# Optimization experiments

Hardware: AMD Instinct MI355X
Metric: run time of the kernel (lower is better)

## Reference

```python
import jax, jax.numpy as jnp
import numpy as np

B, S, HID, NH, HD = 2, 2048, 2048, 16, 128  # batch, seq, hidden, heads, head_dim
ROPE_BASE = 10000.0


def _rope_tables():
    inv_freq = 1.0 / (ROPE_BASE ** (np.arange(0, HD, 2, dtype=np.float64) / HD))
    freqs = np.outer(np.arange(S, dtype=np.float64), inv_freq)  # [S, HD/2]
    emb = np.concatenate([freqs, freqs], axis=-1)  # [S, HD]
    return (jnp.asarray(np.cos(emb), dtype=jnp.float32),
            jnp.asarray(np.sin(emb), dtype=jnp.float32))


def setup_inputs() -> dict:
    key = jax.random.key(0)
    k1, k2, k3 = jax.random.split(key, 3)
    x = jax.random.normal(k1, (B, S, HID), dtype=jnp.float32)
    # CastedLinear init std = 1/sqrt(in_features); plain normal is fine for a numeric reference
    w_qkv = jax.random.normal(k2, (3 * HID, HID), dtype=jnp.float32) * (1.0 / np.sqrt(HID))
    w_o = jax.random.normal(k3, (HID, HID), dtype=jnp.float32) * (1.0 / np.sqrt(HID))
    cos, sin = _rope_tables()
    return {"x": x, "w_qkv": w_qkv, "w_o": w_o, "cos": cos, "sin": sin}


def rotate_half(t):
    t1, t2 = jnp.split(t, 2, axis=-1)
    return jnp.concatenate([-t2, t1], axis=-1)


def reference(x, w_qkv, w_o, cos, sin):
    b, s, _ = x.shape
    # qkv_proj: F.linear -> x @ w_qkv.T
    qkv = jnp.einsum('bsi,oi->bso', x, w_qkv).reshape(b, s, 3, NH, HD)
    q, k, v = qkv[:, :, 0], qkv[:, :, 1], qkv[:, :, 2]  # [b, s, NH, HD]
    # RoPE: cos/sin [s, HD] broadcast over batch and heads
    c = cos[:, None, :]
    sn = sin[:, None, :]
    q = q * c + rotate_half(q) * sn
    k = k * c + rotate_half(k) * sn
    # [b, NH, s, HD]
    q = q.transpose(0, 2, 1, 3)
    k = k.transpose(0, 2, 1, 3)
    v = v.transpose(0, 2, 1, 3)
    scale = 1.0 / jnp.sqrt(jnp.asarray(HD, dtype=x.dtype))
    scores = jnp.einsum('bhqd,bhkd->bhqk', q, k) * scale
    causal_mask = jnp.triu(jnp.ones((s, s), dtype=bool), k=1)
    scores = jnp.where(causal_mask, jnp.asarray(-1e9, dtype=scores.dtype), scores)
    attn = jax.nn.softmax(scores, axis=-1)
    ctx = jnp.einsum('bhqk,bhkd->bhqd', attn, v)
    ctx = ctx.transpose(0, 2, 1, 3).reshape(b, s, HID)
    # o_proj: ctx @ w_o.T
    return jnp.einsum('bsi,oi->bso', ctx, w_o)
```

## Files before the change

### kernel.cpp

```cpp
#include <hip/hip_runtime.h>
#include <hip/hip_bf16.h>

typedef __bf16 bf16;
typedef __bf16 bf16x4 __attribute__((ext_vector_type(4)));
typedef __bf16 bf16x8 __attribute__((ext_vector_type(8)));
typedef float floatx4 __attribute__((ext_vector_type(4)));

#define Bb   2
#define Ss   2048
#define HID  2048
#define NH   16
#define HD   128
#define HG   8

typedef __attribute__((address_space(3))) unsigned int lds_u32;
typedef const __attribute__((address_space(1))) unsigned int gbl_u32;

__device__ __forceinline__ float b2f(bf16 h) {
    unsigned short u = __builtin_bit_cast(unsigned short, h);
    unsigned int x = ((unsigned int)u) << 16;
    return __builtin_bit_cast(float, x);
}
__device__ __forceinline__ bf16 f2b(float f) {
    __hip_bfloat16 t = __float2bfloat16(f);
    return __builtin_bit_cast(bf16, t);
}
__device__ __forceinline__ bf16x8 load8_f32(const float* p) {
    float4 u = *(const float4*)p;
    float4 v = *(const float4*)(p + 4);
    bf16x8 r;
    r[0] = f2b(u.x); r[1] = f2b(u.y); r[2] = f2b(u.z); r[3] = f2b(u.w);
    r[4] = f2b(v.x); r[5] = f2b(v.y); r[6] = f2b(v.z); r[7] = f2b(v.w);
    return r;
}
__device__ __forceinline__ void stage16(const bf16* g, bf16* l) {
    __builtin_amdgcn_global_load_lds((gbl_u32*)g, (lds_u32*)l, 16, 0, 0);
}


__global__ __launch_bounds__(256) void cvt_all(
    const float* __restrict__ x, const float* __restrict__ wq,
    const float* __restrict__ wo,
    bf16* __restrict__ xb, bf16* __restrict__ wqb, bf16* __restrict__ wob)
{
    int idx = blockIdx.x * 256 + threadIdx.x;
    int stride = gridDim.x * 256;
    for (int i = idx; i < 6291456; i += stride) {
        const float* in; bf16* out; int k;
        if (i < 2097152)      { in = x;  out = xb;  k = i; }
        else if (i < 5242880) { in = wq; out = wqb; k = i - 2097152; }
        else                  { in = wo; out = wob; k = i - 5242880; }
        float4 v = ((const float4*)in)[k];
        bf16x4 o; o[0] = f2b(v.x); o[1] = f2b(v.y); o[2] = f2b(v.z); o[3] = f2b(v.w);
        ((bf16x4*)out)[k] = o;
    }
}

__global__ __launch_bounds__(256) void qkv_gemm_rope(
    const bf16* __restrict__ xb, const bf16* __restrict__ wqb,
    const float* __restrict__ c0, const float* __restrict__ c1,
    bf16* __restrict__ q, bf16* __restrict__ k, bf16* __restrict__ vT)
{
    __shared__ __attribute__((aligned(16))) char smem[128 * 132 * 2];
    bf16* As = (bf16*)smem;
    bf16* Bs = (bf16*)(smem + 8192);
    typedef bf16 (*tile_t)[132];
    tile_t tile = (tile_t)smem;

    bool c0cos = (c0[0] > 0.5f);
    const float* cosT = c0cos ? c0 : c1;
    const float* sinT = c0cos ? c1 : c0;

    int tid = threadIdx.x, lane = tid & 63, w = tid >> 6;
    int l15 = lane & 15, quad = lane >> 4;
    int m0 = blockIdx.x * 128, n0 = blockIdx.y * 128;
    int mw = (w >> 1) * 64, nw = (w & 1) * 64;

    int srow = w * 32 + (lane >> 2);
    int scol = (lane & 3) * 8;
    const bf16* ga = xb  + (size_t)(m0 + srow) * HID + scol;
    const bf16* gb = wqb + (size_t)(n0 + srow) * HID + scol;
    bf16* la = As + w * 1024;
    bf16* lb = Bs + w * 1024;

    floatx4 acc[4][4] = {};
    for (int k0 = 0; k0 < HID; k0 += 32) {
        stage16(ga + k0,                    la);
        stage16(ga + (size_t)16 * HID + k0, la + 512);
        stage16(gb + k0,                    lb);
        stage16(gb + (size_t)16 * HID + k0, lb + 512);
        __syncthreads();
        bf16x8 a[4], b[4];
#pragma unroll
        for (int i = 0; i < 4; i++) {
            a[i] = *(const bf16x8*)&As[(mw + i * 16 + l15) * 32 + quad * 8];
            b[i] = *(const bf16x8*)&Bs[(nw + i * 16 + l15) * 32 + quad * 8];
        }
#pragma unroll
        for (int i = 0; i < 4; i++)
#pragma unroll
            for (int j = 0; j < 4; j++)
                acc[i][j] = __builtin_amdgcn_mfma_f32_16x16x32_bf16(a[i], b[j], acc[i][j], 0, 0, 0);
        __syncthreads();
    }

#pragma unroll
    for (int i = 0; i < 4; i++)
#pragma unroll
        for (int j = 0; j < 4; j++) {
            int row_l = mw + i * 16 + quad * 4;
            int col_l = nw + j * 16 + l15;
#pragma unroll
            for (int r = 0; r < 4; r++)
                tile[row_l + r][col_l] = f2b(acc[i][j][r]);
        }
    __syncthreads();

    int sec = blockIdx.y >> 4;
    int h   = blockIdx.y & 15;
    int bi  = m0 >> 11;
    int bh  = bi * NH + h;
    int sbase = m0 & (Ss - 1);

    if (sec == 2) {
        int d  = tid >> 1;
        int sh = (tid & 1) * 64;
        bf16* vrow = vT + ((size_t)bh * HD + d) * Ss + sbase + sh;
#pragma unroll 4
        for (int i = 0; i < 64; i += 4) {
            bf16x4 pk;
#pragma unroll
            for (int r = 0; r < 4; r++) pk[r] = tile[sh + i + r][d];
            *(bf16x4*)(vrow + i) = pk;
        }
    } else {
        bf16* dst = (sec == 0) ? q : k;
        int d  = tid & 63;
        int r0 = tid >> 6;
#pragma unroll 4
        for (int it = 0; it < 32; it++) {
            int row_l = it * 4 + r0;
            int s = sbase + row_l;
            float x1 = b2f(tile[row_l][d]);
            float x2 = b2f(tile[row_l][d + 64]);
            float cc1 = cosT[s * HD + d];
            float ss1 = sinT[s * HD + d];
            float cc2 = cosT[s * HD + d + 64];
            float ss2 = sinT[s * HD + d + 64];
            size_t o = ((size_t)bh * Ss + s) * HD + d;
            dst[o]      = f2b(x1 * cc1 - x2 * ss1);
            dst[o + 64] = f2b(x2 * cc2 + x1 * ss2);
        }
    }
}

#define ATTN_C1 (0.08838834764831845f * 1.44269504f)

#define STAGE_KV(BUF, KB)                                                        \
{                                                                                \
    const char* kg = kgbase + (size_t)(KB) * 256;                                \
    const char* vg = vgbase + (size_t)(KB) * 2;                                  \
    _Pragma("unroll")                                                            \
    for (int i = 0; i < 2; i++) {                                                \
        int P  = P0 + i * 1024;                                                  \
        int r  = P >> 8;                                                         \
        int cK = (P & 255) ^ ((r & 7) << 4);                                     \
        stage16((const bf16*)(kg + r * 256 + cK),                                \
                (bf16*)((char*)Kls[BUF] + wave * 2048 + i * 1024));              \
        int d  = P >> 6;                                                         \
        int cV = (P & 63) ^ (((d >> 1) & 3) << 4);                               \
        stage16((const bf16*)(vg + (size_t)d * 4096 + cV),                       \
                (bf16*)((char*)Vls[BUF] + wave * 2048 + i * 1024));              \
    }                                                                            \
}

__global__ __launch_bounds__(256, 4) void attn_full(
    const bf16* __restrict__ Q, const bf16* __restrict__ Kb, const bf16* __restrict__ VT,
    bf16* __restrict__ O)
{
    __shared__ __attribute__((aligned(16))) bf16 Kls[2][32 * 128];
    __shared__ __attribute__((aligned(16))) bf16 Vls[2][128 * 32];
    __shared__ bf16 pls[4][16][40];

    int id   = blockIdx.x;
    int xcd  = id & 7;
    int j    = id >> 3;
    int bh   = (xcd << 2) | (j & 3);
    int qt   = 31 - (j >> 2);

    int tid  = threadIdx.x;
    int wave = tid >> 6;
    int lane = tid & 63;
    int l15  = lane & 15;
    int quad = lane >> 4;

    int q0 = qt * 64 + wave * 16;
    int qg = q0 + l15;

    const char* kgbase = (const char*)(Kb + (size_t)bh * Ss * HD);
    const char* vgbase = (const char*)(VT + (size_t)bh * HD * Ss);
    int P0 = wave * 2048 + lane * 16;

    STAGE_KV(0, 0);

    const bf16* qptr = Q + ((size_t)bh * Ss + qg) * HD + quad * 8;
    bf16x8 qf[4];
#pragma unroll
    for (int s = 0; s < 4; s++) qf[s] = *(const bf16x8*)(qptr + s * 32);

    float m    = -1e30f;
    float bm   = 1.44269504e30f;
    float lsum = 0.0f;
    floatx4 ctx[8] = {};

    int nsteps = 2 * qt + 2;
    int buf = 0;
    __syncthreads();

    for (int st = 0; st < nsteps; st++) {
        int kb = st * 32;
        if (st + 1 < nsteps) {
            int bufn = buf ^ 1;
            STAGE_KV(bufn, kb + 32);
        }
        if (kb <= q0 + 15) {
            bool masked = (kb + 31 > q0);
            const char* kls = (const char*)Kls[buf];
            const char* vls = (const char*)Vls[buf];

            floatx4 s0 = {0.f,0.f,0.f,0.f}, s1 = {0.f,0.f,0.f,0.f};
            __builtin_amdgcn_s_setprio(1);
#pragma unroll
            for (int s = 0; s < 4; s++) {
                int c = (quad * 16 + s * 64) ^ ((l15 & 7) << 4);
                bf16x8 k0 = *(const bf16x8*)(kls + l15 * 256 + c);
                bf16x8 k1 = *(const bf16x8*)(kls + (l15 + 16) * 256 + c);
                s0 = __builtin_amdgcn_mfma_f32_16x16x32_bf16(k0, qf[s], s0, 0, 0, 0);
                s1 = __builtin_amdgcn_mfma_f32_16x16x32_bf16(k1, qf[s], s1, 0, 0, 0);
            }
            __builtin_amdgcn_s_setprio(0);

            float v0[4], v1[4];
#pragma unroll
            for (int r = 0; r < 4; r++) {
                int key0 = kb + quad * 4 + r;
                v0[r] = (masked && key0 > qg)      ? -1e9f : s0[r];
                v1[r] = (masked && key0 + 16 > qg) ? -1e9f : s1[r];
            }
            float lmax = fmaxf(fmaxf(fmaxf(v0[0], v0[1]), fmaxf(v0[2], v0[3])),
                               fmaxf(fmaxf(v1[0], v1[1]), fmaxf(v1[2], v1[3])));
            if (!__all(lmax * 0.08838834764831845f <= m + 8.0f)) {
                float tm = lmax;
                tm = fmaxf(tm, __shfl_xor(tm, 16));
                tm = fmaxf(tm, __shfl_xor(tm, 32));
                float tms  = tm * 0.08838834764831845f;
                float mnew = fmaxf(m, tms);
                float bmn  = -mnew * 1.44269504f;
                float alpha = __builtin_exp2f(bmn - bm);
                m = mnew; bm = bmn;
                lsum *= alpha;
#pragma unroll
                for (int t = 0; t < 8; t++) {
                    ctx[t][0] *= alpha; ctx[t][1] *= alpha;
                    ctx[t][2] *= alpha; ctx[t][3] *= alpha;
                }
            }
            bf16x4 pk0, pk1; float ts = 0.f;
#pragma unroll
            for (int r = 0; r < 4; r++) {
                float pe0 = __builtin_exp2f(__builtin_fmaf(v0[r], ATTN_C1, bm));
                float pe1 = __builtin_exp2f(__builtin_fmaf(v1[r], ATTN_C1, bm));
                ts += pe0 + pe1;
                pk0[r] = f2b(pe0); pk1[r] = f2b(pe1);
            }
            lsum += ts;
            *(bf16x4*)&pls[wave][l15][quad * 4]      = pk0;
            *(bf16x4*)&pls[wave][l15][16 + quad * 4] = pk1;
            bf16x8 pf = *(const bf16x8*)&pls[wave][l15][quad * 8];

            __builtin_amdgcn_s_setprio(1);
#pragma unroll
            for (int t = 0; t < 8; t++) {
                int row = t * 16 + l15;
                bf16x8 vf = *(const bf16x8*)(vls + row * 64 +
                                             ((quad * 16) ^ (((row >> 1) & 3) << 4)));
                ctx[t] = __builtin_amdgcn_mfma_f32_16x16x32_bf16(vf, pf, ctx[t], 0, 0, 0);
            }
            __builtin_amdgcn_s_setprio(0);
        }
        __syncthreads();
        buf ^= 1;
    }

    lsum += __shfl_xor(lsum, 16);
    lsum += __shfl_xor(lsum, 32);
    float inv = 1.0f / lsum;

    int bi = bh >> 4, h = bh & (NH - 1);
    bf16* op = O + ((size_t)(bi * Ss + qg)) * HID + h * HD;
#pragma unroll
    for (int t = 0; t < 8; t++) {
        bf16x4 ov;
#pragma unroll
        for (int r = 0; r < 4; r++) ov[r] = f2b(ctx[t][r] * inv);
        *(bf16x4*)(op + t * 16 + quad * 4) = ov;
    }
}

__global__ __launch_bounds__(256) void out_gemm(
    const bf16* __restrict__ A, const bf16* __restrict__ B, float* __restrict__ C)
{
    __shared__ bf16 As[128 * 32];
    __shared__ bf16 Bs[128 * 32];

    int tid = threadIdx.x, lane = tid & 63, w = tid >> 6;
    int l15 = lane & 15, quad = lane >> 4;
    int m0 = blockIdx.x * 128, n0 = blockIdx.y * 128;
    int mw = (w >> 1) * 64, nw = (w & 1) * 64;

    int srow = w * 32 + (lane >> 2);
    int scol = (lane & 3) * 8;
    const bf16* ga = A + (size_t)(m0 + srow) * HID + scol;
    const bf16* gb = B + (size_t)(n0 + srow) * HID + scol;
    bf16* la = As + w * 1024;
    bf16* lb = Bs + w * 1024;

    floatx4 acc[4][4] = {};
    for (int k0 = 0; k0 < HID; k0 += 32) {
        stage16(ga + k0,                    la);
        stage16(ga + (size_t)16 * HID + k0, la + 512);
        stage16(gb + k0,                    lb);
        stage16(gb + (size_t)16 * HID + k0, lb + 512);
        __syncthreads();
        bf16x8 a[4], b[4];
#pragma unroll
        for (int i = 0; i < 4; i++) {
            a[i] = *(const bf16x8*)&As[(mw + i * 16 + l15) * 32 + quad * 8];
            b[i] = *(const bf16x8*)&Bs[(nw + i * 16 + l15) * 32 + quad * 8];
        }
#pragma unroll
        for (int i = 0; i < 4; i++)
#pragma unroll
            for (int j = 0; j < 4; j++)
                acc[i][j] = __builtin_amdgcn_mfma_f32_16x16x32_bf16(a[i], b[j], acc[i][j], 0, 0, 0);
        __syncthreads();
    }

#pragma unroll
    for (int i = 0; i < 4; i++)
#pragma unroll
        for (int j = 0; j < 4; j++) {
            int row = m0 + mw + i * 16 + quad * 4;
            int col = n0 + nw + j * 16 + l15;
#pragma unroll
            for (int r = 0; r < 4; r++)
                C[(size_t)(row + r) * HID + col] = acc[i][j][r];
        }
}


__global__ __launch_bounds__(256) void qkv_rope_pass(
    const float* __restrict__ xb, const float* __restrict__ W,
    const float* __restrict__ c0, const float* __restrict__ c1,
    bf16* __restrict__ qc, bf16* __restrict__ kc, bf16* __restrict__ vc, int hg)
{
    __shared__ bf16 tile[128][132];
    bool c0cos = (c0[0] > 0.5f);
    const float* cosT = c0cos ? c0 : c1;
    const float* sinT = c0cos ? c1 : c0;

    int tid = threadIdx.x, lane = tid & 63, wave = tid >> 6;
    int l15 = lane & 15, quad = lane >> 4;
    int sec = blockIdx.y >> 3, hl = blockIdx.y & 7;
    int nbase = sec * (NH * HD) + (hg * HG + hl) * HD;
    int m0 = blockIdx.x * 128 + (wave >> 1) * 64;
    int n0l = (wave & 1) * 64;

    floatx4 acc[4][4] = {};
    const float* ap = xb + (size_t)(m0 + l15) * HID + quad * 8;
    const float* bp = W  + (size_t)(nbase + n0l + l15) * HID + quad * 8;
    for (int k0 = 0; k0 < HID; k0 += 32) {
        bf16x8 a[4], b[4];
#pragma unroll
        for (int i = 0; i < 4; i++) {
            a[i] = load8_f32(ap + (size_t)i * 16 * HID + k0);
            b[i] = load8_f32(bp + (size_t)i * 16 * HID + k0);
        }
#pragma unroll
        for (int i = 0; i < 4; i++)
#pragma unroll
            for (int j = 0; j < 4; j++)
                acc[i][j] = __builtin_amdgcn_mfma_f32_16x16x32_bf16(a[i], b[j], acc[i][j], 0, 0, 0);
    }
    int lr = (wave >> 1) * 64;
#pragma unroll
    for (int i = 0; i < 4; i++)
#pragma unroll
        for (int j = 0; j < 4; j++) {
            int row_l = lr + i * 16 + quad * 4;
            int col_l = n0l + j * 16 + l15;
#pragma unroll
            for (int r = 0; r < 4; r++)
                tile[row_l + r][col_l] = f2b(acc[i][j][r]);
        }
    __syncthreads();

    bf16* dst = (sec == 0) ? qc : (sec == 1) ? kc : vc;
    int d = tid & 63, r0 = tid >> 6;
#pragma unroll 4
    for (int it = 0; it < 32; it++) {
        int row_l = it * 4 + r0;
        int s = blockIdx.x * 128 + row_l;
        float x1 = b2f(tile[row_l][d]);
        float x2 = b2f(tile[row_l][d + 64]);
        size_t o = ((size_t)hl * Ss + s) * HD + d;
        if (sec == 2) { dst[o] = f2b(x1); dst[o + 64] = f2b(x2); }
        else {
            float cc1 = cosT[s * HD + d], ss1 = sinT[s * HD + d];
            float cc2 = cosT[s * HD + d + 64], ss2 = sinT[s * HD + d + 64];
            dst[o]      = f2b(x1 * cc1 - x2 * ss1);
            dst[o + 64] = f2b(x2 * cc2 + x1 * ss2);
        }
    }
}

__global__ __launch_bounds__(256) void attn_pass(
    const bf16* __restrict__ Q, const bf16* __restrict__ Kb, const bf16* __restrict__ Vb,
    bf16* __restrict__ Obase)
{
    __shared__ bf16 pls[4][16][40];
    int hl = blockIdx.x;
    int qt = (gridDim.y - 1) - blockIdx.y;
    int tid = threadIdx.x, wave = tid >> 6, lane = tid & 63;
    int l15 = lane & 15, quad = lane >> 4;
    int q0 = qt * 64 + wave * 16;
    int qg = q0 + l15;

    const bf16* qptr = Q + ((size_t)hl * Ss + qg) * HD + quad * 8;
    bf16x8 qf[4];
#pragma unroll
    for (int s = 0; s < 4; s++) qf[s] = *(const bf16x8*)(qptr + s * 32);

    float m = -1e30f, l = 0.0f;
    floatx4 ctx[8] = {};
    const float scale = 0.08838834764831845f;

    for (int kb = 0; kb <= q0 + 15; kb += 32) {
        floatx4 s0 = {0.f,0.f,0.f,0.f}, s1 = {0.f,0.f,0.f,0.f};
        const bf16* kp0 = Kb + ((size_t)hl * Ss + kb + l15) * HD + quad * 8;
        const bf16* kp1 = kp0 + (size_t)16 * HD;
#pragma unroll
        for (int s = 0; s < 4; s++) {
            bf16x8 k0 = *(const bf16x8*)(kp0 + s * 32);
            bf16x8 k1 = *(const bf16x8*)(kp1 + s * 32);
            s0 = __builtin_amdgcn_mfma_f32_16x16x32_bf16(k0, qf[s], s0, 0, 0, 0);
            s1 = __builtin_amdgcn_mfma_f32_16x16x32_bf16(k1, qf[s], s1, 0, 0, 0);
        }
        float v0[4], v1[4];
#pragma unroll
        for (int r = 0; r < 4; r++) {
            int key0 = kb + quad * 4 + r;
            v0[r] = (key0 > qg)      ? -1e9f : s0[r] * scale;
            v1[r] = (key0 + 16 > qg) ? -1e9f : s1[r] * scale;
        }
        float tmax = fmaxf(fmaxf(fmaxf(v0[0], v0[1]), fmaxf(v0[2], v0[3])),
                           fmaxf(fmaxf(v1[0], v1[1]), fmaxf(v1[2], v1[3])));
        tmax = fmaxf(tmax, __shfl_xor(tmax, 16));
        tmax = fmaxf(tmax, __shfl_xor(tmax, 32));
        float mnew = fmaxf(m, tmax);
        float alpha = __expf(m - mnew);
        float p0[4], p1[4], tsum = 0.0f;
#pragma unroll
        for (int r = 0; r < 4; r++) {
            p0[r] = __expf(v0[r] - mnew);
            p1[r] = __expf(v1[r] - mnew);
            tsum += p0[r] + p1[r];
        }
        tsum += __shfl_xor(tsum, 16);
        tsum += __shfl_xor(tsum, 32);
        l = l * alpha + tsum;
        m = mnew;
#pragma unroll
        for (int t = 0; t < 8; t++) {
            ctx[t][0] *= alpha; ctx[t][1] *= alpha;
            ctx[t][2] *= alpha; ctx[t][3] *= alpha;
        }
#pragma unroll
        for (int r = 0; r < 4; r++) {
            pls[wave][l15][quad * 4 + r]      = f2b(p0[r]);
            pls[wave][l15][16 + quad * 4 + r] = f2b(p1[r]);
        }
        bf16x8 pf = *(const bf16x8*)&pls[wave][l15][quad * 8];
        const short* vp = (const short*)(Vb + ((size_t)hl * Ss + kb) * HD);
#pragma unroll
        for (int t = 0; t < 8; t++) {
            bf16x8 vf;
#pragma unroll
            for (int j = 0; j < 8; j++) {
                short sv = vp[(size_t)(quad * 8 + j) * HD + t * 16 + l15];
                vf[j] = __builtin_bit_cast(bf16, sv);
            }
            ctx[t] = __builtin_amdgcn_mfma_f32_16x16x32_bf16(vf, pf, ctx[t], 0, 0, 0);
        }
    }
    float inv = 1.0f / l;
    bf16* op = Obase + (size_t)qg * HID + hl * HD;
#pragma unroll
    for (int t = 0; t < 8; t++) {
        bf16x4 ov;
#pragma unroll
        for (int r = 0; r < 4; r++) ov[r] = f2b(ctx[t][r] * inv);
        *(bf16x4*)(op + t * 16 + quad * 4) = ov;
    }
}

__global__ __launch_bounds__(256) void gemm_out_f32(
    const bf16* __restrict__ A, const float* __restrict__ B,
    float* __restrict__ C, int N, int K)
{
    int tid = threadIdx.x, lane = tid & 63, wave = tid >> 6;
    int l15 = lane & 15, quad = lane >> 4;
    int m0 = blockIdx.x * 128 + (wave >> 1) * 64;
    int n0 = blockIdx.y * 128 + (wave & 1) * 64;

    floatx4 acc[4][4] = {};
    const bf16*  ap = A + (size_t)(m0 + l15) * K + quad * 8;
    const float* bp = B + (size_t)(n0 + l15) * K + quad * 8;
    for (int k0 = 0; k0 < K; k0 += 32) {
        bf16x8 a[4], b[4];
#pragma unroll
        for (int i = 0; i < 4; i++) {
            a[i] = *(const bf16x8*)(ap + (size_t)i * 16 * K + k0);
            b[i] = load8_f32(bp + (size_t)i * 16 * K + k0);
        }
#pragma unroll
        for (int i = 0; i < 4; i++)
#pragma unroll
            for (int j = 0; j < 4; j++)
                acc[i][j] = __builtin_amdgcn_mfma_f32_16x16x32_bf16(a[i], b[j], acc[i][j], 0, 0, 0);
    }
#pragma unroll
    for (int i = 0; i < 4; i++)
#pragma unroll
        for (int j = 0; j < 4; j++) {
            int row = m0 + i * 16 + quad * 4;
            int col = n0 + j * 16 + l15;
#pragma unroll
            for (int r = 0; r < 4; r++)
                C[(size_t)(row + r) * N + col] = acc[i][j][r];
        }
}

extern "C" void kernel_launch(void* const* d_in, const int* in_sizes, int n_in,
                              void* d_out, int out_size, void* d_ws, size_t ws_size,
                              hipStream_t stream)
{
    const float *x = nullptr, *w_qkv = nullptr, *w_o = nullptr;
    const float *t0 = nullptr, *t1 = nullptr;
    for (int i = 0; i < n_in; i++) {
        const float* p = (const float*)d_in[i];
        if      (in_sizes[i] == 12582912) w_qkv = p;
        else if (in_sizes[i] ==  8388608) x     = p;
        else if (in_sizes[i] ==  4194304) w_o   = p;
        else if (in_sizes[i] ==   262144) { if (t0) t1 = p; else t0 = p; }
    }
    float* out = (float*)d_out;
    char* ws = (char*)d_ws;

    if (ws_size >= (size_t)67108864) {
        bf16* xb  = (bf16*)ws;
        bf16* wqb = (bf16*)(ws + 16777216);
        bf16* wob = (bf16*)(ws + 41943040);
        bf16* ctx = (bf16*)ws;
        bf16 *qb, *kbuf, *vT;
        if (ws_size >= (size_t)100663296) {
            qb   = (bf16*)(ws + 50331648);
            kbuf = (bf16*)(ws + 67108864);
            vT   = (bf16*)(ws + 83886080);
        } else {
            qb   = (bf16*)d_out;
            kbuf = (bf16*)((char*)d_out + 16777216);
            vT   = (bf16*)(ws + 50331648);
        }

        cvt_all<<<2048, 256, 0, stream>>>(x, w_qkv, w_o, xb, wqb, wob);

        qkv_gemm_rope<<<dim3(32, 48), 256, 0, stream>>>(xb, wqb, t0, t1, qb, kbuf, vT);
        attn_full<<<dim3(1024), 256, 0, stream>>>(qb, kbuf, vT, ctx);
        out_gemm<<<dim3(32, 16), 256, 0, stream>>>(ctx, wob, out);
    } else {
        const size_t pe = (size_t)HG * Ss * HD;
        bf16* qc = (bf16*)d_ws;
        bf16* kc = qc + pe;
        bf16* vc = kc + pe;
        float* fin = (float*)d_ws;
        bf16* ctx = (bf16*)((char*)d_out + (size_t)16777216);

        for (int bi = 0; bi < Bb; bi++) {
            const float* xbp = x + (size_t)bi * Ss * HID;
            for (int hg = 0; hg < 2; hg++) {
                qkv_rope_pass<<<dim3(Ss / 128, 24), 256, 0, stream>>>(
                    xbp, w_qkv, t0, t1, qc, kc, vc, hg);
                bf16* Obase = ctx + (size_t)bi * Ss * HID + (size_t)hg * HG * HD;
                attn_pass<<<dim3(HG, Ss / 64), 256, 0, stream>>>(qc, kc, vc, Obase);
            }
        }
        gemm_out_f32<<<dim3(16, 16), 256, 0, stream>>>(ctx, w_o, fin, HID, HID);
        hipMemcpyAsync(out, fin, (size_t)2048 * HID * sizeof(float),
                       hipMemcpyDeviceToDevice, stream);
        gemm_out_f32<<<dim3(16, 16), 256, 0, stream>>>(ctx + (size_t)2048 * HID, w_o,
                                                       fin, HID, HID);
        hipMemcpyAsync(out + (size_t)2048 * HID, fin, (size_t)2048 * HID * sizeof(float),
                       hipMemcpyDeviceToDevice, stream);
    }
}
```

Before: 380.5 us.

## Double attention query tile so each wave processes two 16-row subtiles

The causal attention kernel now gives each block 128 queries, and each wave handles 32 query rows as two 16-row subtiles. Every K/V fragment read from LDS feeds two MFMAs instead of one, which halves LDS traffic and K/V staging per query. The grid drops from 1024 to 512 blocks, with a new block-to-(head, query-tile) mapping that balances causal work, and launch bounds are relaxed to 2 blocks per CU. In exchange it uses many more registers and runs fewer, longer blocks, which can hurt latency hiding and tail balance.

```diff
diff --git a/kernel.cpp b/kernel.cpp
--- a/kernel.cpp
+++ b/kernel.cpp
@@ -174,19 +174,19 @@
     }                                                                            \
 }
 
-__global__ __launch_bounds__(256, 4) void attn_full(
+__global__ __launch_bounds__(256, 2) void attn_full(
     const bf16* __restrict__ Q, const bf16* __restrict__ Kb, const bf16* __restrict__ VT,
     bf16* __restrict__ O)
 {
     __shared__ __attribute__((aligned(16))) bf16 Kls[2][32 * 128];
     __shared__ __attribute__((aligned(16))) bf16 Vls[2][128 * 32];
-    __shared__ bf16 pls[4][16][40];
+    __shared__ bf16 pls[4][2][16][40];
 
     int id   = blockIdx.x;
     int xcd  = id & 7;
     int j    = id >> 3;
     int bh   = (xcd << 2) | (j & 3);
-    int qt   = 31 - (j >> 2);
+    int qt   = (id < 256) ? (15 - (id >> 5)) : ((id >> 5) - 8);
 
     int tid  = threadIdx.x;
     int wave = tid >> 6;
@@ -194,7 +194,7 @@
     int l15  = lane & 15;
     int quad = lane >> 4;
 
-    int q0 = qt * 64 + wave * 16;
+    int q0 = qt * 128 + wave * 32;
     int qg = q0 + l15;
 
     const char* kgbase = (const char*)(Kb + (size_t)bh * Ss * HD);
@@ -204,79 +204,105 @@
     STAGE_KV(0, 0);
 
     const bf16* qptr = Q + ((size_t)bh * Ss + qg) * HD + quad * 8;
-    bf16x8 qf[4];
-#pragma unroll
-    for (int s = 0; s < 4; s++) qf[s] = *(const bf16x8*)(qptr + s * 32);
-
-    float m    = -1e30f;
-    float bm   = 1.44269504e30f;
-    float lsum = 0.0f;
-    floatx4 ctx[8] = {};
-
-    int nsteps = 2 * qt + 2;
+    bf16x8 qf0[4], qf1[4];
+#pragma unroll
+    for (int s = 0; s < 4; s++) {
+        qf0[s] = *(const bf16x8*)(qptr + s * 32);
+        qf1[s] = *(const bf16x8*)(qptr + (size_t)16 * HD + s * 32);
+    }
+
+    float m0v = -1e30f, m1v = -1e30f;
+    float bm0 = 1.44269504e30f, bm1 = 1.44269504e30f;
+    float ls0 = 0.0f, ls1 = 0.0f;
+    floatx4 ctx0[8] = {}, ctx1[8] = {};
+
+    int nsteps = 4 * qt + 4;
     int buf = 0;
     __syncthreads();
 
     for (int st = 0; st < nsteps; st++) {
         int kb = st * 32;
         if (st + 1 < nsteps) {
-            int bufn = buf ^ 1;
-            STAGE_KV(bufn, kb + 32);
-        }
-        if (kb <= q0 + 15) {
-            bool masked = (kb + 31 > q0);
+            STAGE_KV(buf ^ 1, kb + 32);
+        }
+        if (kb <= q0) {
+            bool masked = (kb == q0);
             const char* kls = (const char*)Kls[buf];
             const char* vls = (const char*)Vls[buf];
 
             floatx4 s0 = {0.f,0.f,0.f,0.f}, s1 = {0.f,0.f,0.f,0.f};
+            floatx4 s2 = {0.f,0.f,0.f,0.f}, s3 = {0.f,0.f,0.f,0.f};
             __builtin_amdgcn_s_setprio(1);
 #pragma unroll
             for (int s = 0; s < 4; s++) {
                 int c = (quad * 16 + s * 64) ^ ((l15 & 7) << 4);
                 bf16x8 k0 = *(const bf16x8*)(kls + l15 * 256 + c);
                 bf16x8 k1 = *(const bf16x8*)(kls + (l15 + 16) * 256 + c);
-                s0 = __builtin_amdgcn_mfma_f32_16x16x32_bf16(k0, qf[s], s0, 0, 0, 0);
-                s1 = __builtin_amdgcn_mfma_f32_16x16x32_bf16(k1, qf[s], s1, 0, 0, 0);
+                s0 = __builtin_amdgcn_mfma_f32_16x16x32_bf16(k0, qf0[s], s0, 0, 0, 0);
+                s1 = __builtin_amdgcn_mfma_f32_16x16x32_bf16(k1, qf0[s], s1, 0, 0, 0);
+                s2 = __builtin_amdgcn_mfma_f32_16x16x32_bf16(k0, qf1[s], s2, 0, 0, 0);
+                s3 = __builtin_amdgcn_mfma_f32_16x16x32_bf16(k1, qf1[s], s3, 0, 0, 0);
             }
             __builtin_amdgcn_s_setprio(0);
 
-            float v0[4], v1[4];
+            float v00[4], v01[4], v10[4], v11[4];
 #pragma unroll
             for (int r = 0; r < 4; r++) {
                 int key0 = kb + quad * 4 + r;
-                v0[r] = (masked && key0 > qg)      ? -1e9f : s0[r];
-                v1[r] = (masked && key0 + 16 > qg) ? -1e9f : s1[r];
+                v00[r] = (masked && key0 > qg)           ? -1e9f : s0[r];
+                v01[r] = (masked && key0 + 16 > qg)      ? -1e9f : s1[r];
+                v10[r] = (masked && key0 > qg + 16)      ? -1e9f : s2[r];
+                v11[r] = (masked && key0 + 16 > qg + 16) ? -1e9f : s3[r];
             }
-            float lmax = fmaxf(fmaxf(fmaxf(v0[0], v0[1]), fmaxf(v0[2], v0[3])),
-                               fmaxf(fmaxf(v1[0], v1[1]), fmaxf(v1[2], v1[3])));
-            if (!__all(lmax * 0.08838834764831845f <= m + 8.0f)) {
-                float tm = lmax;
-                tm = fmaxf(tm, __shfl_xor(tm, 16));
-                tm = fmaxf(tm, __shfl_xor(tm, 32));
-                float tms  = tm * 0.08838834764831845f;
-                float mnew = fmaxf(m, tms);
-                float bmn  = -mnew * 1.44269504f;
-                float alpha = __builtin_exp2f(bmn - bm);
-                m = mnew; bm = bmn;
-                lsum *= alpha;
+            float lmax0 = fmaxf(fmaxf(fmaxf(v00[0], v00[1]), fmaxf(v00[2], v00[3])),
+                                fmaxf(fmaxf(v01[0], v01[1]), fmaxf(v01[2], v01[3])));
+            float lmax1 = fmaxf(fmaxf(fmaxf(v10[0], v10[1]), fmaxf(v10[2], v10[3])),
+                                fmaxf(fmaxf(v11[0], v11[1]), fmaxf(v11[2], v11[3])));
+            bool ok = (lmax0 * 0.08838834764831845f <= m0v + 8.0f) &&
+                      (lmax1 * 0.08838834764831845f <= m1v + 8.0f);
+            if (!__all(ok)) {
+                float tm0 = lmax0, tm1 = lmax1;
+                tm0 = fmaxf(tm0, __shfl_xor(tm0, 16));
+                tm0 = fmaxf(tm0, __shfl_xor(tm0, 32));
+                tm1 = fmaxf(tm1, __shfl_xor(tm1, 16));
+                tm1 = fmaxf(tm1, __shfl_xor(tm1, 32));
+                float mnew0 = fmaxf(m0v, tm0 * 0.08838834764831845f);
+                float mnew1 = fmaxf(m1v, tm1 * 0.08838834764831845f);
+                float bmn0 = -mnew0 * 1.44269504f;
+                float bmn1 = -mnew1 * 1.44269504f;
+                float a0 = __builtin_exp2f(bmn0 - bm0);
+                float a1 = __builtin_exp2f(bmn1 - bm1);
+                m0v = mnew0; bm0 = bmn0; ls0 *= a0;
+                m1v = mnew1; bm1 = bmn1; ls1 *= a1;
 #pragma unroll
                 for (int t = 0; t < 8; t++) {
-                    ctx[t][0] *= alpha; ctx[t][1] *= alpha;
-                    ctx[t][2] *= alpha; ctx[t][3] *= alpha;
+                    ctx0[t][0] *= a0; ctx0[t][1] *= a0;
+                    ctx0[t][2] *= a0; ctx0[t][3] *= a0;
+                    ctx1[t][0] *= a1; ctx1[t][1] *= a1;
+                    ctx1[t][2] *= a1; ctx1[t][3] *= a1;
                 }
             }
-            bf16x4 pk0, pk1; float ts = 0.f;
+            bf16x4 pk00, pk01, pk10, pk11;
+            float ts0 = 0.f, ts1 = 0.f;
 #pragma unroll
             for (int r = 0; r < 4; r++) {
-                float pe0 = __builtin_exp2f(__builtin_fmaf(v0[r], ATTN_C1, bm));
-                float pe1 = __builtin_exp2f(__builtin_fmaf(v1[r], ATTN_C1, bm));
-                ts += pe0 + pe1;
-                pk0[r] = f2b(pe0); pk1[r] = f2b(pe1);
+                float pe00 = __builtin_exp2f(__builtin_fmaf(v00[r], ATTN_C1, bm0));
+                float pe01 = __builtin_exp2f(__builtin_fmaf(v01[r], ATTN_C1, bm0));
+                float pe10 = __builtin_exp2f(__builtin_fmaf(v10[r], ATTN_C1, bm1));
+                float pe11 = __builtin_exp2f(__builtin_fmaf(v11[r], ATTN_C1, bm1));
+                ts0 += pe00 + pe01;
+                ts1 += pe10 + pe11;
+                pk00[r] = f2b(pe00); pk01[r] = f2b(pe01);
+                pk10[r] = f2b(pe10); pk11[r] = f2b(pe11);
             }
-            lsum += ts;
-            *(bf16x4*)&pls[wave][l15][quad * 4]      = pk0;
-            *(bf16x4*)&pls[wave][l15][16 + quad * 4] = pk1;
-            bf16x8 pf = *(const bf16x8*)&pls[wave][l15][quad * 8];
+            ls0 += ts0;
+            ls1 += ts1;
+            *(bf16x4*)&pls[wave][0][l15][quad * 4]      = pk00;
+            *(bf16x4*)&pls[wave][0][l15][16 + quad * 4] = pk01;
+            *(bf16x4*)&pls[wave][1][l15][quad * 4]      = pk10;
+            *(bf16x4*)&pls[wave][1][l15][16 + quad * 4] = pk11;
+            bf16x8 pf0 = *(const bf16x8*)&pls[wave][0][l15][quad * 8];
+            bf16x8 pf1 = *(const bf16x8*)&pls[wave][1][l15][quad * 8];
 
             __builtin_amdgcn_s_setprio(1);
 #pragma unroll
@@ -284,7 +310,8 @@
                 int row = t * 16 + l15;
                 bf16x8 vf = *(const bf16x8*)(vls + row * 64 +
                                              ((quad * 16) ^ (((row >> 1) & 3) << 4)));
-                ctx[t] = __builtin_amdgcn_mfma_f32_16x16x32_bf16(vf, pf, ctx[t], 0, 0, 0);
+                ctx0[t] = __builtin_amdgcn_mfma_f32_16x16x32_bf16(vf, pf0, ctx0[t], 0, 0, 0);
+                ctx1[t] = __builtin_amdgcn_mfma_f32_16x16x32_bf16(vf, pf1, ctx1[t], 0, 0, 0);
             }
             __builtin_amdgcn_s_setprio(0);
         }
@@ -292,18 +319,26 @@
         buf ^= 1;
     }
 
-    lsum += __shfl_xor(lsum, 16);
-    lsum += __shfl_xor(lsum, 32);
-    float inv = 1.0f / lsum;
+    ls0 += __shfl_xor(ls0, 16);
+    ls0 += __shfl_xor(ls0, 32);
+    ls1 += __shfl_xor(ls1, 16);
+    ls1 += __shfl_xor(ls1, 32);
+    float inv0 = 1.0f / ls0;
+    float inv1 = 1.0f / ls1;
 
     int bi = bh >> 4, h = bh & (NH - 1);
-    bf16* op = O + ((size_t)(bi * Ss + qg)) * HID + h * HD;
+    bf16* op0 = O + ((size_t)(bi * Ss + qg)) * HID + h * HD;
+    bf16* op1 = op0 + (size_t)16 * HID;
 #pragma unroll
     for (int t = 0; t < 8; t++) {
-        bf16x4 ov;
-#pragma unroll
-        for (int r = 0; r < 4; r++) ov[r] = f2b(ctx[t][r] * inv);
-        *(bf16x4*)(op + t * 16 + quad * 4) = ov;
+        bf16x4 ov0, ov1;
+#pragma unroll
+        for (int r = 0; r < 4; r++) {
+            ov0[r] = f2b(ctx0[t][r] * inv0);
+            ov1[r] = f2b(ctx1[t][r] * inv1);
+        }
+        *(bf16x4*)(op0 + t * 16 + quad * 4) = ov0;
+        *(bf16x4*)(op1 + t * 16 + quad * 4) = ov1;
     }
 }
 
@@ -586,7 +621,7 @@
         cvt_all<<<2048, 256, 0, stream>>>(x, w_qkv, w_o, xb, wqb, wob);
 
         qkv_gemm_rope<<<dim3(32, 48), 256, 0, stream>>>(xb, wqb, t0, t1, qb, kbuf, vT);
-        attn_full<<<dim3(1024), 256, 0, stream>>>(qb, kbuf, vT, ctx);
+        attn_full<<<dim3(512), 256, 0, stream>>>(qb, kbuf, vT, ctx);
         out_gemm<<<dim3(32, 16), 256, 0, stream>>>(ctx, wob, out);
     } else {
         const size_t pe = (size_t)HG * Ss * HD;
```

Result: slower. 402.8 us (+5.9%).
